# Performance work log

Hardware: AMD Instinct MI355X
Metric: run time of the kernel (lower is better)

The kernel has to match this reference:

```python
import jax, jax.numpy as jnp
import numpy as np

N = 100000
E = 1600000
DIMS = [128, 128, 64]


def _gcn_norm(edge_index, num_nodes):
    # PyG gcn_norm: add self-loops, symmetric normalization D^-1/2 (A+I) D^-1/2
    src, dst = edge_index[0], edge_index[1]
    loop = jnp.arange(num_nodes, dtype=src.dtype)
    src = jnp.concatenate([src, loop])
    dst = jnp.concatenate([dst, loop])
    deg = jax.ops.segment_sum(jnp.ones_like(src, dtype=jnp.float32), dst,
                              num_segments=num_nodes)
    dinv = jnp.where(deg > 0, jax.lax.rsqrt(deg), 0.0)
    w = dinv[src] * dinv[dst]  # [E+N]
    return src, dst, w


def _gcn_conv(x, src, dst, w, W, b):
    # transform first (cheaper when out_dim <= in_dim), then aggregate
    h = x @ W                                   # [N, out]
    msg = h[src] * w[:, None]                   # gather + scale  [E+N, out]
    out = jax.ops.segment_sum(msg, dst, num_segments=x.shape[0])
    return out + b


def setup_inputs() -> dict:
    key = jax.random.key(0)
    ks = jax.random.split(key, 6)
    x = jax.random.normal(ks[0], (N, DIMS[0]), dtype=jnp.float32)
    edge_index = jax.random.randint(ks[1], (2, E), 0, N, dtype=jnp.int64)
    # Glorot-style init for GCNConv weights, zero bias (PyG default)
    W1 = jax.random.normal(ks[2], (DIMS[0], DIMS[1]), dtype=jnp.float32) / np.sqrt(DIMS[0])
    b1 = jnp.zeros((DIMS[1],), dtype=jnp.float32)
    W2 = jax.random.normal(ks[3], (DIMS[1], DIMS[2]), dtype=jnp.float32) / np.sqrt(DIMS[1])
    b2 = jnp.zeros((DIMS[2],), dtype=jnp.float32)
    return {"x": x, "edge_index": edge_index, "W1": W1, "b1": b1, "W2": W2, "b2": b2}


def reference(x, edge_index, W1, b1, W2, b2):
    src, dst, w = _gcn_norm(edge_index, x.shape[0])
    h = _gcn_conv(x, src, dst, w, W1, b1)
    h = jax.nn.relu(h)
    # dropout is identity in eval mode (deterministic reference)
    out = _gcn_conv(h, src, dst, w, W2, b2)
    return out
```

## Files before the change

kernel.cpp:

```cpp
#include <hip/hip_runtime.h>
#include <hip/hip_fp16.h>

#define TPB 256
#define CHUNK 1024
#define EPB 4096
#define CSHIFT 8
#define AGG_BLOCKS 2048

typedef _Float16 half8 __attribute__((ext_vector_type(8)));
typedef float    f32x4 __attribute__((ext_vector_type(4)));


__global__ __launch_bounds__(256) void scanA_kernel(const int* __restrict__ cnt,
                                                    int* __restrict__ row_ptr,
                                                    int* __restrict__ chunk_sums, int n) {
    __shared__ int ls[256];
    const int t    = threadIdx.x;
    const int base = blockIdx.x * CHUNK;
    const int idx  = base + t * 4;
    int4 v = make_int4(0, 0, 0, 0);
    if (idx + 3 < n) v = *(const int4*)(cnt + idx);
    else {
        if (idx + 0 < n) v.x = cnt[idx + 0];
        if (idx + 1 < n) v.y = cnt[idx + 1];
        if (idx + 2 < n) v.z = cnt[idx + 2];
        if (idx + 3 < n) v.w = cnt[idx + 3];
    }
    int s0 = v.x, s1 = s0 + v.y, s2 = s1 + v.z, s3 = s2 + v.w;
    ls[t] = s3;
    __syncthreads();
    for (int off = 1; off < 256; off <<= 1) {
        int xv = (t >= off) ? ls[t - off] : 0;
        __syncthreads();
        ls[t] += xv;
        __syncthreads();
    }
    int excl = (t == 0) ? 0 : ls[t - 1];
    if (idx + 0 < n) row_ptr[idx + 0] = excl;
    if (idx + 1 < n) row_ptr[idx + 1] = excl + s0;
    if (idx + 2 < n) row_ptr[idx + 2] = excl + s1;
    if (idx + 3 < n) row_ptr[idx + 3] = excl + s2;
    if (t == 255) chunk_sums[blockIdx.x] = ls[255];
}

__global__ __launch_bounds__(256) void scanB_kernel(int* __restrict__ chunk_sums, int nch) {
    __shared__ int ls[256];
    const int t = threadIdx.x;
    ls[t] = (t < nch) ? chunk_sums[t] : 0;
    __syncthreads();
    for (int off = 1; off < 256; off <<= 1) {
        int xv = (t >= off) ? ls[t - off] : 0;
        __syncthreads();
        ls[t] += xv;
        __syncthreads();
    }
    if (t < nch) chunk_sums[t] = (t == 0) ? 0 : ls[t - 1];
}


__global__ __launch_bounds__(256) void hist_kernel(const int* __restrict__ dst,
                                                   int* __restrict__ hist_g,
                                                   int e, int nbc, int nblk) {
    __shared__ int hs[512];
    const int t = threadIdx.x;
    for (int i = t; i < nbc; i += 256) hs[i] = 0;
    __syncthreads();
    const int e0  = blockIdx.x * EPB;
    const int lim = min(e0 + EPB, e);
    for (int i = e0 + t; i < lim; i += 256)
        atomicAdd(&hs[dst[i] >> CSHIFT], 1);
    __syncthreads();
    for (int b = t; b < nbc; b += 256)
        hist_g[b * nblk + blockIdx.x] = hs[b];
}

__global__ __launch_bounds__(256) void partition_kernel(const int* __restrict__ src,
                                                        const int* __restrict__ dst,
                                                        const int* __restrict__ hist_scan,
                                                        const int* __restrict__ chunk_sums,
                                                        int* __restrict__ pairs,
                                                        int e, int nbc, int nblk) {
    __shared__ int  hs[512];
    __shared__ int  lscan[512];
    __shared__ int  lfill[512];
    __shared__ int  base_s[512];
    __shared__ int  ls[256];
    __shared__ int2 sp[EPB];
    const int t = threadIdx.x;
    for (int i = t; i < nbc; i += 256) { hs[i] = 0; lfill[i] = 0; }
    __syncthreads();
    const int e0  = blockIdx.x * EPB;
    const int lim = min(e0 + EPB, e);
    for (int i = e0 + t; i < lim; i += 256)
        atomicAdd(&hs[dst[i] >> CSHIFT], 1);
    __syncthreads();
    int v0 = (2 * t     < nbc) ? hs[2 * t]     : 0;
    int v1 = (2 * t + 1 < nbc) ? hs[2 * t + 1] : 0;
    ls[t] = v0 + v1;
    __syncthreads();
    for (int off = 1; off < 256; off <<= 1) {
        int xv = (t >= off) ? ls[t - off] : 0;
        __syncthreads();
        ls[t] += xv;
        __syncthreads();
    }
    int excl = (t == 0) ? 0 : ls[t - 1];
    if (2 * t     < nbc) lscan[2 * t]     = excl;
    if (2 * t + 1 < nbc) lscan[2 * t + 1] = excl + v0;
    for (int b = t; b < nbc; b += 256) {
        int hidx = b * nblk + blockIdx.x;
        base_s[b] = hist_scan[hidx] + chunk_sums[hidx >> 10];
    }
    __syncthreads();
    for (int i = e0 + t; i < lim; i += 256) {
        int d = dst[i];
        int b = d >> CSHIFT;
        int r = atomicAdd(&lfill[b], 1);
        sp[lscan[b] + r] = make_int2(src[i], d);
    }
    __syncthreads();
    const int cnt = lim - e0;
    for (int i = t; i < cnt; i += 256) {
        int2 pr = sp[i];
        int  b  = pr.y >> CSHIFT;
        pairs[base_s[b] + (i - lscan[b])] = pr.x | ((pr.y & 255) << 17);
    }
}

__global__ __launch_bounds__(256) void bucket_finalize_kernel(const int* __restrict__ pairs,
                                                              const int* __restrict__ hist_scan,
                                                              const int* __restrict__ chunk_sums,
                                                              int* __restrict__ row_ptr,
                                                              float* __restrict__ dinv,
                                                              int* __restrict__ csr_src,
                                                              int n, int e, int nbc, int nblk) {
    __shared__ int cnt_s[256];
    __shared__ int fill[256];
    __shared__ int ls[256];
    const int b   = blockIdx.x;
    const int nb0 = b << CSHIFT;
    const int t   = threadIdx.x;
    const int h0  = b * nblk;
    const int r0  = hist_scan[h0] + chunk_sums[h0 >> 10];
    int r1 = e;
    if (b + 1 < nbc) {
        const int h1 = (b + 1) * nblk;
        r1 = hist_scan[h1] + chunk_sums[h1 >> 10];
    }
    cnt_s[t] = 0;
    __syncthreads();
    for (int i = r0 + t; i < r1; i += 256)
        atomicAdd(&cnt_s[pairs[i] >> 17], 1);
    __syncthreads();
    int c = cnt_s[t];
    ls[t] = c;
    __syncthreads();
    for (int off = 1; off < 256; off <<= 1) {
        int xv = (t >= off) ? ls[t - off] : 0;
        __syncthreads();
        ls[t] += xv;
        __syncthreads();
    }
    int excl = (t == 0) ? 0 : ls[t - 1];
    int node = nb0 + t;
    if (node < n) {
        row_ptr[node] = r0 + excl;
        dinv[node]    = rsqrtf((float)(c + 1));
    }
    fill[t] = r0 + excl;
    __syncthreads();
    for (int i = r0 + t; i < r1; i += 256) {
        int pr = pairs[i];
        int p  = atomicAdd(&fill[pr >> 17], 1);
        csr_src[p] = pr & 0x1FFFF;
    }
    if (b == 0 && t == 0) row_ptr[n] = e;
}


__global__ __launch_bounds__(256) void wprep_kernel(const float* __restrict__ W1,
                                                    const float* __restrict__ W2,
                                                    _Float16* __restrict__ wf1g,
                                                    _Float16* __restrict__ wf2g) {
    const int tid = threadIdx.x;
    if (blockIdx.x == 0) {
        for (int f = tid; f < 8 * 4 * 64; f += 256) {
            int c    = f >> 8;
            int i    = (f >> 6) & 3;
            int lane = f & 63;
            int quad = lane >> 4, n = lane & 15;
            const float* wp = W1 + (size_t)(i * 32 + quad * 8) * 128 + c * 16 + n;
            half8 hv;
#pragma unroll
            for (int j = 0; j < 8; ++j) hv[j] = (_Float16)wp[(size_t)j * 128];
            ((half8*)wf1g)[f] = hv;
        }
    } else {
        for (int f = tid; f < 4 * 4 * 64; f += 256) {
            int c    = f >> 8;
            int i    = (f >> 6) & 3;
            int lane = f & 63;
            int quad = lane >> 4, n = lane & 15;
            const float* wp = W2 + (size_t)(i * 32 + quad * 8) * 64 + c * 16 + n;
            half8 hv;
#pragma unroll
            for (int j = 0; j < 8; ++j) hv[j] = (_Float16)wp[(size_t)j * 64];
            ((half8*)wf2g)[f] = hv;
        }
    }
}


template <int M, bool RELU, typename XT>
__global__ __launch_bounds__(256) void gemm_mfma_kernel(const XT* __restrict__ X,
                                                        const _Float16* __restrict__ Wfg,
                                                        const float* __restrict__ dinv,
                                                        __half* __restrict__ H, int nrows) {
    constexpr int NC = M / 16;
    __shared__ __align__(16) _Float16 Wf[NC * 4 * 64 * 8];

    const int tid = threadIdx.x;
    const uint4* wb = (const uint4*)Wfg;
    for (int f = tid; f < NC * 4 * 64; f += 256)
        ((uint4*)Wf)[f] = wb[f];
    __syncthreads();

    const int  wave = tid >> 6, lane = tid & 63;
    const int  quad = lane >> 4, n16 = lane & 15;
    const long rowbase = (long)blockIdx.x * 64 + wave * 16;

    long arow = rowbase + n16;
    const XT* xrow = X + (size_t)(arow < nrows ? arow : 0) * 128;
    half8 a[4];
    if constexpr (sizeof(XT) == 4) {
        const float4* xr = (const float4*)xrow;
#pragma unroll
        for (int i = 0; i < 4; ++i) {
            float4 x0 = xr[i * 8 + quad * 2];
            float4 x1 = xr[i * 8 + quad * 2 + 1];
            if (RELU) {
                x0.x = fmaxf(x0.x, 0.f); x0.y = fmaxf(x0.y, 0.f);
                x0.z = fmaxf(x0.z, 0.f); x0.w = fmaxf(x0.w, 0.f);
                x1.x = fmaxf(x1.x, 0.f); x1.y = fmaxf(x1.y, 0.f);
                x1.z = fmaxf(x1.z, 0.f); x1.w = fmaxf(x1.w, 0.f);
            }
            half8 hv;
            hv[0] = (_Float16)x0.x; hv[1] = (_Float16)x0.y;
            hv[2] = (_Float16)x0.z; hv[3] = (_Float16)x0.w;
            hv[4] = (_Float16)x1.x; hv[5] = (_Float16)x1.y;
            hv[6] = (_Float16)x1.z; hv[7] = (_Float16)x1.w;
            a[i] = hv;
        }
    } else {
        const half8* xr = (const half8*)xrow;
#pragma unroll
        for (int i = 0; i < 4; ++i) {
            half8 hv = xr[i * 4 + quad];
            if (RELU) {
#pragma unroll
                for (int j = 0; j < 8; ++j)
                    hv[j] = (hv[j] > (_Float16)0) ? hv[j] : (_Float16)0;
            }
            a[i] = hv;
        }
    }

    float dv[4];
#pragma unroll
    for (int r = 0; r < 4; ++r) {
        long orow = rowbase + quad * 4 + r;
        dv[r] = (orow < nrows) ? dinv[orow] : 0.f;
    }

    for (int c = 0; c < NC; ++c) {
        f32x4 acc = {0.f, 0.f, 0.f, 0.f};
#pragma unroll
        for (int i = 0; i < 4; ++i) {
            half8 b = ((const half8*)Wf)[(c * 4 + i) * 64 + lane];
            acc = __builtin_amdgcn_mfma_f32_16x16x32_f16(a[i], b, acc, 0, 0, 0);
        }
#pragma unroll
        for (int r = 0; r < 4; ++r) {
            long orow = rowbase + quad * 4 + r;
            if (orow < nrows)
                H[orow * M + c * 16 + n16] = __float2half(acc[r] * dv[r]);
        }
    }
}


__device__ __forceinline__ void add_u4(float2* a, const uint4& u) {
    float2 v0 = __half22float2(*(const __half2*)&u.x);
    float2 v1 = __half22float2(*(const __half2*)&u.y);
    float2 v2 = __half22float2(*(const __half2*)&u.z);
    float2 v3 = __half22float2(*(const __half2*)&u.w);
    a[0].x += v0.x; a[0].y += v0.y;
    a[1].x += v1.x; a[1].y += v1.y;
    a[2].x += v2.x; a[2].y += v2.y;
    a[3].x += v3.x; a[3].y += v3.y;
}


__global__ __launch_bounds__(TPB) void agg_pull128_kernel(const __half* __restrict__ hs,
                                                          const int* __restrict__ csr_src,
                                                          const int* __restrict__ row_ptr,
                                                          const float* __restrict__ dinv,
                                                          const float* __restrict__ bias,
                                                          __half* __restrict__ out, int n) {
    const int wid  = blockIdx.x * (TPB / 64) + (threadIdx.x >> 6);
    const int NW   = gridDim.x * (TPB / 64);
    const int lane = threadIdx.x & 63;
    const int q    = lane >> 4;
    const int sl   = lane & 15;
    if (wid >= n) return;
    const uint4* up   = (const uint4*)hs;
    const uint4* upsl = up + sl;

    const float4* bp = (const float4*)bias;
    const float4 bb0 = bp[2 * sl], bb1 = bp[2 * sl + 1];

    int b0 = row_ptr[wid], e0 = row_ptr[wid + 1];
    int nA = wid + NW;
    int b1 = 0, e1 = 0;
    if (nA < n) { b1 = row_ptr[nA]; e1 = row_ptr[nA + 1]; }
    int m0 = e0 - b0; if (m0 > 64) m0 = 64;
    int idx0 = (lane < m0) ? csr_src[b0 + lane] : 0;
    uint4 self0 = make_uint4(0, 0, 0, 0);
    if (q == 0) self0 = up[(size_t)wid * 16 + sl];
    float dv0 = dinv[wid];

    for (int ni = wid; ni < n; ni += NW) {
        const int n1 = ni + NW, n2 = ni + 2 * NW;
        int b2 = 0, e2 = 0;
        if (n2 < n) { b2 = row_ptr[n2]; e2 = row_ptr[n2 + 1]; }
        int idx1 = 0; uint4 self1 = make_uint4(0, 0, 0, 0); float dv1 = 0.f;
        if (n1 < n) {
            int m1 = e1 - b1; if (m1 > 64) m1 = 64;
            idx1 = (lane < m1) ? csr_src[b1 + lane] : 0;
            if (q == 0) self1 = up[(size_t)n1 * 16 + sl];
            dv1 = dinv[n1];
        }
        int m = e0 - b0; if (m > 64) m = 64;
        int sA0 = __shfl(idx0, q);
        int sA1 = __shfl(idx0, 4 + q);
        int sA2 = __shfl(idx0, 8 + q);
        int sA3 = __shfl(idx0, 12 + q);
        int sB0 = __shfl(idx0, 16 + q);
        int sB1 = __shfl(idx0, 20 + q);
        int sB2 = __shfl(idx0, 24 + q);
        int sB3 = __shfl(idx0, 28 + q);
        uint4 uA0 = upsl[(size_t)(unsigned)sA0 * 16];
        uint4 uA1 = upsl[(size_t)(unsigned)sA1 * 16];
        uint4 uA2 = upsl[(size_t)(unsigned)sA2 * 16];
        uint4 uA3 = upsl[(size_t)(unsigned)sA3 * 16];
        uint4 uB0 = upsl[(size_t)(unsigned)sB0 * 16];
        uint4 uB1 = upsl[(size_t)(unsigned)sB1 * 16];
        uint4 uB2 = upsl[(size_t)(unsigned)sB2 * 16];
        uint4 uB3 = upsl[(size_t)(unsigned)sB3 * 16];
        float2 a0[4], a1[4];
#pragma unroll
        for (int k = 0; k < 4; ++k) { a0[k] = make_float2(0.f, 0.f); a1[k] = make_float2(0.f, 0.f); }
        if (m >= 32) {
            add_u4(a0, uA0); add_u4(a1, uA1); add_u4(a0, uA2); add_u4(a1, uA3);
            add_u4(a0, uB0); add_u4(a1, uB1); add_u4(a0, uB2); add_u4(a1, uB3);
        } else {
            if (q < m)      add_u4(a0, uA0);
            if (4 + q < m)  add_u4(a1, uA1);
            if (8 + q < m)  add_u4(a0, uA2);
            if (12 + q < m) add_u4(a1, uA3);
            if (16 + q < m) add_u4(a0, uB0);
            if (20 + q < m) add_u4(a1, uB1);
            if (24 + q < m) add_u4(a0, uB2);
            if (28 + q < m) add_u4(a1, uB3);
        }
        for (int j = 32; j < m; j += 16) {
            int s0 = __shfl(idx0, j + q);
            int s1 = __shfl(idx0, j + 4 + q);
            int s2 = __shfl(idx0, j + 8 + q);
            int s3 = __shfl(idx0, j + 12 + q);
            uint4 u0 = upsl[(size_t)(unsigned)s0 * 16];
            uint4 u1 = upsl[(size_t)(unsigned)s1 * 16];
            uint4 u2 = upsl[(size_t)(unsigned)s2 * 16];
            uint4 u3 = upsl[(size_t)(unsigned)s3 * 16];
            if (j + q < m)      add_u4(a0, u0);
            if (j + 4 + q < m)  add_u4(a1, u1);
            if (j + 8 + q < m)  add_u4(a0, u2);
            if (j + 12 + q < m) add_u4(a1, u3);
        }
        for (int base = b0 + 64; base < e0; base += 64) {
            int mm = e0 - base; if (mm > 64) mm = 64;
            int idxv = (lane < mm) ? csr_src[base + lane] : 0;
            for (int j = 0; j < mm; j += 16) {
                int s0 = __shfl(idxv, j + q);
                int s1 = __shfl(idxv, j + 4 + q);
                int s2 = __shfl(idxv, j + 8 + q);
                int s3 = __shfl(idxv, j + 12 + q);
                uint4 u0 = upsl[(size_t)(unsigned)s0 * 16];
                uint4 u1 = upsl[(size_t)(unsigned)s1 * 16];
                uint4 u2 = upsl[(size_t)(unsigned)s2 * 16];
                uint4 u3 = upsl[(size_t)(unsigned)s3 * 16];
                if (j + q < mm)      add_u4(a0, u0);
                if (j + 4 + q < mm)  add_u4(a1, u1);
                if (j + 8 + q < mm)  add_u4(a0, u2);
                if (j + 12 + q < mm) add_u4(a1, u3);
            }
        }
#pragma unroll
        for (int k = 0; k < 4; ++k) { a0[k].x += a1[k].x; a0[k].y += a1[k].y; }
#pragma unroll
        for (int k = 0; k < 4; ++k) {
            a0[k].x += __shfl(a0[k].x, lane ^ 16);
            a0[k].y += __shfl(a0[k].y, lane ^ 16);
            a0[k].x += __shfl(a0[k].x, lane ^ 32);
            a0[k].y += __shfl(a0[k].y, lane ^ 32);
        }
        if (q == 0) {
            float2 v0 = __half22float2(*(const __half2*)&self0.x);
            float2 v1 = __half22float2(*(const __half2*)&self0.y);
            float2 v2 = __half22float2(*(const __half2*)&self0.z);
            float2 v3 = __half22float2(*(const __half2*)&self0.w);
            __half2 h0 = __floats2half2_rn(bb0.x + dv0 * (a0[0].x + v0.x),
                                           bb0.y + dv0 * (a0[0].y + v0.y));
            __half2 h1 = __floats2half2_rn(bb0.z + dv0 * (a0[1].x + v1.x),
                                           bb0.w + dv0 * (a0[1].y + v1.y));
            __half2 h2 = __floats2half2_rn(bb1.x + dv0 * (a0[2].x + v2.x),
                                           bb1.y + dv0 * (a0[2].y + v2.y));
            __half2 h3 = __floats2half2_rn(bb1.z + dv0 * (a0[3].x + v3.x),
                                           bb1.w + dv0 * (a0[3].y + v3.y));
            uint4 ov;
            ov.x = *(const unsigned*)&h0; ov.y = *(const unsigned*)&h1;
            ov.z = *(const unsigned*)&h2; ov.w = *(const unsigned*)&h3;
            ((uint4*)out)[(size_t)ni * 16 + sl] = ov;
        }
        b0 = b1; e0 = e1; idx0 = idx1; self0 = self1; dv0 = dv1;
        b1 = b2; e1 = e2;
    }
}


__global__ __launch_bounds__(TPB) void agg_pull64_kernel(const __half* __restrict__ hs,
                                                         const int* __restrict__ csr_src,
                                                         const int* __restrict__ row_ptr,
                                                         const float* __restrict__ dinv,
                                                         const float* __restrict__ bias,
                                                         float* __restrict__ out, int n) {
    const int wid  = blockIdx.x * (TPB / 64) + (threadIdx.x >> 6);
    const int NW   = gridDim.x * (TPB / 64);
    const int lane = threadIdx.x & 63;
    const int q    = lane >> 3;
    const int sl   = lane & 7;
    if (wid >= n) return;
    const uint4* up   = (const uint4*)hs;
    const uint4* upsl = up + sl;

    const float4* bp = (const float4*)bias;
    const float4 bb0 = bp[2 * sl], bb1 = bp[2 * sl + 1];

    int b0 = row_ptr[wid], e0 = row_ptr[wid + 1];
    int nA = wid + NW;
    int b1 = 0, e1 = 0;
    if (nA < n) { b1 = row_ptr[nA]; e1 = row_ptr[nA + 1]; }
    int m0 = e0 - b0; if (m0 > 64) m0 = 64;
    int idx0 = (lane < m0) ? csr_src[b0 + lane] : 0;
    uint4 self0 = make_uint4(0, 0, 0, 0);
    if (q == 0) self0 = up[(size_t)wid * 8 + sl];
    float dv0 = dinv[wid];

    for (int ni = wid; ni < n; ni += NW) {
        const int n1 = ni + NW, n2 = ni + 2 * NW;
        int b2 = 0, e2 = 0;
        if (n2 < n) { b2 = row_ptr[n2]; e2 = row_ptr[n2 + 1]; }
        int idx1 = 0; uint4 self1 = make_uint4(0, 0, 0, 0); float dv1 = 0.f;
        if (n1 < n) {
            int m1 = e1 - b1; if (m1 > 64) m1 = 64;
            idx1 = (lane < m1) ? csr_src[b1 + lane] : 0;
            if (q == 0) self1 = up[(size_t)n1 * 8 + sl];
            dv1 = dinv[n1];
        }
        int m = e0 - b0; if (m > 64) m = 64;
        int sA0 = __shfl(idx0, q);
        int sA1 = __shfl(idx0, 8 + q);
        int sB0 = __shfl(idx0, 16 + q);
        int sB1 = __shfl(idx0, 24 + q);
        uint4 uA0 = upsl[(size_t)(unsigned)sA0 * 8];
        uint4 uA1 = upsl[(size_t)(unsigned)sA1 * 8];
        uint4 uB0 = upsl[(size_t)(unsigned)sB0 * 8];
        uint4 uB1 = upsl[(size_t)(unsigned)sB1 * 8];
        float2 a0[4], a1[4];
#pragma unroll
        for (int k = 0; k < 4; ++k) { a0[k] = make_float2(0.f, 0.f); a1[k] = make_float2(0.f, 0.f); }
        if (m >= 32) {
            add_u4(a0, uA0); add_u4(a1, uA1); add_u4(a0, uB0); add_u4(a1, uB1);
        } else {
            if (q < m)      add_u4(a0, uA0);
            if (8 + q < m)  add_u4(a1, uA1);
            if (16 + q < m) add_u4(a0, uB0);
            if (24 + q < m) add_u4(a1, uB1);
        }
        for (int j = 32; j < m; j += 16) {
            int s0 = __shfl(idx0, j + q);
            int s1 = __shfl(idx0, j + 8 + q);
            uint4 u0 = upsl[(size_t)(unsigned)s0 * 8];
            uint4 u1 = upsl[(size_t)(unsigned)s1 * 8];
            if (j + q < m)     add_u4(a0, u0);
            if (j + 8 + q < m) add_u4(a1, u1);
        }
        for (int base = b0 + 64; base < e0; base += 64) {
            int mm = e0 - base; if (mm > 64) mm = 64;
            int idxv = (lane < mm) ? csr_src[base + lane] : 0;
            for (int j = 0; j < mm; j += 16) {
                int s0 = __shfl(idxv, j + q);
                int s1 = __shfl(idxv, j + 8 + q);
                uint4 u0 = upsl[(size_t)(unsigned)s0 * 8];
                uint4 u1 = upsl[(size_t)(unsigned)s1 * 8];
                if (j + q < mm)     add_u4(a0, u0);
                if (j + 8 + q < mm) add_u4(a1, u1);
            }
        }
#pragma unroll
        for (int k = 0; k < 4; ++k) { a0[k].x += a1[k].x; a0[k].y += a1[k].y; }
#pragma unroll
        for (int k = 0; k < 4; ++k) {
            a0[k].x += __shfl(a0[k].x, lane ^ 8);
            a0[k].y += __shfl(a0[k].y, lane ^ 8);
            a0[k].x += __shfl(a0[k].x, lane ^ 16);
            a0[k].y += __shfl(a0[k].y, lane ^ 16);
            a0[k].x += __shfl(a0[k].x, lane ^ 32);
            a0[k].y += __shfl(a0[k].y, lane ^ 32);
        }
        if (q == 0) {
            float2 v0 = __half22float2(*(const __half2*)&self0.x);
            float2 v1 = __half22float2(*(const __half2*)&self0.y);
            float2 v2 = __half22float2(*(const __half2*)&self0.z);
            float2 v3 = __half22float2(*(const __half2*)&self0.w);
            float4 o0, o1;
            o0.x = bb0.x + dv0 * (a0[0].x + v0.x);
            o0.y = bb0.y + dv0 * (a0[0].y + v0.y);
            o0.z = bb0.z + dv0 * (a0[1].x + v1.x);
            o0.w = bb0.w + dv0 * (a0[1].y + v1.y);
            o1.x = bb1.x + dv0 * (a0[2].x + v2.x);
            o1.y = bb1.y + dv0 * (a0[2].y + v2.y);
            o1.z = bb1.z + dv0 * (a0[3].x + v3.x);
            o1.w = bb1.w + dv0 * (a0[3].y + v3.y);
            ((float4*)out)[(size_t)ni * 16 + 2 * sl]     = o0;
            ((float4*)out)[(size_t)ni * 16 + 2 * sl + 1] = o1;
        }
        b0 = b1; e0 = e1; idx0 = idx1; self0 = self1; dv0 = dv1;
        b1 = b2; e1 = e2;
    }
}


extern "C" void kernel_launch(void* const* d_in, const int* in_sizes, int n_in,
                              void* d_out, int out_size, void* d_ws, size_t ws_size,
                              hipStream_t stream) {
    const float* x  = (const float*)d_in[0];
    const int*   ei = (const int*)d_in[1];
    const float* W1 = (const float*)d_in[2];
    const float* b1 = (const float*)d_in[3];
    const float* W2 = (const float*)d_in[4];
    const float* b2 = (const float*)d_in[5];
    float* out = (float*)d_out;

    const int N = in_sizes[0] / 128;
    const int E = in_sizes[1] / 2;
    const int* srcv = ei;
    const int* dstv = ei + E;

    const int NBC    = (N + 255) >> CSHIFT;
    const int NBLK_E = (E + EPB - 1) / EPB;
    const int HLEN   = NBC * NBLK_E;
    const int NCHH   = (HLEN + CHUNK - 1) / CHUNK;

    char* p = (char*)d_ws;
    int*      row_ptr    = (int*)p;      p += (((size_t)N + 64) * 4 + 63) & ~(size_t)63;
    int*      chunk_sums = (int*)p;      p += 1024;
    int*      hist       = (int*)p;      p += (((size_t)HLEN + 64) * 4 + 63) & ~(size_t)63;
    int*      csr_src    = (int*)p;      p += ((size_t)E * 4 + 63) & ~(size_t)63;
    float*    dinv       = (float*)p;    p += (((size_t)N + 64) * 4 + 63) & ~(size_t)63;
    _Float16* wf1g       = (_Float16*)p; p += 8 * 4 * 64 * 16;
    _Float16* wf2g       = (_Float16*)p; p += 4 * 4 * 64 * 16;
    __half*   hs1        = (__half*)p;   p += (size_t)N * 128 * 2;
    __half*   out1       = (__half*)p;   p += (size_t)N * 128 * 2;
    int*      pairs      = (int*)out1;
    __half*   hs2        = hs1;

    wprep_kernel<<<2, 256, 0, stream>>>(W1, W2, wf1g, wf2g);

    hist_kernel<<<NBLK_E, 256, 0, stream>>>(dstv, hist, E, NBC, NBLK_E);
    scanA_kernel<<<NCHH, 256, 0, stream>>>(hist, hist, chunk_sums, HLEN);
    scanB_kernel<<<1, 256, 0, stream>>>(chunk_sums, NCHH);
    partition_kernel<<<NBLK_E, 256, 0, stream>>>(srcv, dstv, hist, chunk_sums, pairs,
                                                 E, NBC, NBLK_E);
    bucket_finalize_kernel<<<NBC, 256, 0, stream>>>(pairs, hist, chunk_sums, row_ptr, dinv,
                                                    csr_src, N, E, NBC, NBLK_E);

    gemm_mfma_kernel<128, false, float><<<(N + 63) / 64, 256, 0, stream>>>(x, wf1g, dinv, hs1, N);
    agg_pull128_kernel<<<AGG_BLOCKS, TPB, 0, stream>>>(hs1, csr_src, row_ptr, dinv, b1, out1, N);

    gemm_mfma_kernel<64, true, _Float16><<<(N + 63) / 64, 256, 0, stream>>>(
        (const _Float16*)out1, wf2g, dinv, hs2, N);
    agg_pull64_kernel<<<AGG_BLOCKS, TPB, 0, stream>>>(hs2, csr_src, row_ptr, dinv, b2, out, N);
}
```

Measured before the change: 270.8 us.

## Fuse CSR build and first GEMM into one persistent kernel with grid barriers

Merges weight prep, histogram, scans, partition, bucket finalize and the first MFMA GEMM into a single kernel that uses software grid barriers built on global atomics. It also changes the histogram scan to a per-bucket layout, so two scan kernels become in-block scans. The aim is to remove several kernel launches and the gaps between them. In exchange the GEMM now runs on only max(NBC, NBLK_E) ≈ 391 blocks looping over tiles instead of about 1563 blocks, and the barriers assume every block is resident at once, which can deadlock if it is not.

```diff
diff --git a/kernel.cpp b/kernel.cpp
--- a/kernel.cpp
+++ b/kernel.cpp
@@ -2,7 +2,6 @@
 #include <hip/hip_fp16.h>
 
 #define TPB 256
-#define CHUNK 1024
 #define EPB 4096
 #define CSHIFT 8
 #define AGG_BLOCKS 2048
@@ -11,91 +10,23 @@
 typedef float    f32x4 __attribute__((ext_vector_type(4)));
 
 
-__global__ __launch_bounds__(256) void scanA_kernel(const int* __restrict__ cnt,
-                                                    int* __restrict__ row_ptr,
-                                                    int* __restrict__ chunk_sums, int n) {
-    __shared__ int ls[256];
-    const int t    = threadIdx.x;
-    const int base = blockIdx.x * CHUNK;
-    const int idx  = base + t * 4;
-    int4 v = make_int4(0, 0, 0, 0);
-    if (idx + 3 < n) v = *(const int4*)(cnt + idx);
-    else {
-        if (idx + 0 < n) v.x = cnt[idx + 0];
-        if (idx + 1 < n) v.y = cnt[idx + 1];
-        if (idx + 2 < n) v.z = cnt[idx + 2];
-        if (idx + 3 < n) v.w = cnt[idx + 3];
-    }
-    int s0 = v.x, s1 = s0 + v.y, s2 = s1 + v.z, s3 = s2 + v.w;
-    ls[t] = s3;
+__device__ __forceinline__ void grid_barrier(int* bar, int id, int nblk) {
     __syncthreads();
-    for (int off = 1; off < 256; off <<= 1) {
-        int xv = (t >= off) ? ls[t - off] : 0;
-        __syncthreads();
-        ls[t] += xv;
-        __syncthreads();
-    }
-    int excl = (t == 0) ? 0 : ls[t - 1];
-    if (idx + 0 < n) row_ptr[idx + 0] = excl;
-    if (idx + 1 < n) row_ptr[idx + 1] = excl + s0;
-    if (idx + 2 < n) row_ptr[idx + 2] = excl + s1;
-    if (idx + 3 < n) row_ptr[idx + 3] = excl + s2;
-    if (t == 255) chunk_sums[blockIdx.x] = ls[255];
-}
-
-__global__ __launch_bounds__(256) void scanB_kernel(int* __restrict__ chunk_sums, int nch) {
-    __shared__ int ls[256];
+    if (threadIdx.x == 0) {
+        __threadfence();
+        __hip_atomic_fetch_add(&bar[id], 1, __ATOMIC_RELEASE, __HIP_MEMORY_SCOPE_AGENT);
+        while (__hip_atomic_load(&bar[id], __ATOMIC_ACQUIRE, __HIP_MEMORY_SCOPE_AGENT) < nblk)
+            __builtin_amdgcn_s_sleep(4);
+        __threadfence();
+    }
+    __syncthreads();
+}
+
+__device__ __forceinline__ void scan512_global(int* a, int len, int* ls, int* total_out) {
     const int t = threadIdx.x;
-    ls[t] = (t < nch) ? chunk_sums[t] : 0;
-    __syncthreads();
-    for (int off = 1; off < 256; off <<= 1) {
-        int xv = (t >= off) ? ls[t - off] : 0;
-        __syncthreads();
-        ls[t] += xv;
-        __syncthreads();
-    }
-    if (t < nch) chunk_sums[t] = (t == 0) ? 0 : ls[t - 1];
-}
-
-
-__global__ __launch_bounds__(256) void hist_kernel(const int* __restrict__ dst,
-                                                   int* __restrict__ hist_g,
-                                                   int e, int nbc, int nblk) {
-    __shared__ int hs[512];
-    const int t = threadIdx.x;
-    for (int i = t; i < nbc; i += 256) hs[i] = 0;
-    __syncthreads();
-    const int e0  = blockIdx.x * EPB;
-    const int lim = min(e0 + EPB, e);
-    for (int i = e0 + t; i < lim; i += 256)
-        atomicAdd(&hs[dst[i] >> CSHIFT], 1);
-    __syncthreads();
-    for (int b = t; b < nbc; b += 256)
-        hist_g[b * nblk + blockIdx.x] = hs[b];
-}
-
-__global__ __launch_bounds__(256) void partition_kernel(const int* __restrict__ src,
-                                                        const int* __restrict__ dst,
-                                                        const int* __restrict__ hist_scan,
-                                                        const int* __restrict__ chunk_sums,
-                                                        int* __restrict__ pairs,
-                                                        int e, int nbc, int nblk) {
-    __shared__ int  hs[512];
-    __shared__ int  lscan[512];
-    __shared__ int  lfill[512];
-    __shared__ int  base_s[512];
-    __shared__ int  ls[256];
-    __shared__ int2 sp[EPB];
-    const int t = threadIdx.x;
-    for (int i = t; i < nbc; i += 256) { hs[i] = 0; lfill[i] = 0; }
-    __syncthreads();
-    const int e0  = blockIdx.x * EPB;
-    const int lim = min(e0 + EPB, e);
-    for (int i = e0 + t; i < lim; i += 256)
-        atomicAdd(&hs[dst[i] >> CSHIFT], 1);
-    __syncthreads();
-    int v0 = (2 * t     < nbc) ? hs[2 * t]     : 0;
-    int v1 = (2 * t + 1 < nbc) ? hs[2 * t + 1] : 0;
+    const int i0 = 2 * t, i1 = 2 * t + 1;
+    int v0 = (i0 < len) ? a[i0] : 0;
+    int v1 = (i1 < len) ? a[i1] : 0;
     ls[t] = v0 + v1;
     __syncthreads();
     for (int off = 1; off < 256; off <<= 1) {
@@ -105,107 +36,201 @@
         __syncthreads();
     }
     int excl = (t == 0) ? 0 : ls[t - 1];
-    if (2 * t     < nbc) lscan[2 * t]     = excl;
-    if (2 * t + 1 < nbc) lscan[2 * t + 1] = excl + v0;
-    for (int b = t; b < nbc; b += 256) {
-        int hidx = b * nblk + blockIdx.x;
-        base_s[b] = hist_scan[hidx] + chunk_sums[hidx >> 10];
-    }
+    if (i0 < len) a[i0] = excl;
+    if (i1 < len) a[i1] = excl + v0;
+    if (t == 255 && total_out) *total_out = ls[255];
     __syncthreads();
-    for (int i = e0 + t; i < lim; i += 256) {
-        int d = dst[i];
-        int b = d >> CSHIFT;
-        int r = atomicAdd(&lfill[b], 1);
-        sp[lscan[b] + r] = make_int2(src[i], d);
-    }
-    __syncthreads();
-    const int cnt = lim - e0;
-    for (int i = t; i < cnt; i += 256) {
-        int2 pr = sp[i];
-        int  b  = pr.y >> CSHIFT;
-        pairs[base_s[b] + (i - lscan[b])] = pr.x | ((pr.y & 255) << 17);
-    }
-}
-
-__global__ __launch_bounds__(256) void bucket_finalize_kernel(const int* __restrict__ pairs,
-                                                              const int* __restrict__ hist_scan,
-                                                              const int* __restrict__ chunk_sums,
-                                                              int* __restrict__ row_ptr,
-                                                              float* __restrict__ dinv,
-                                                              int* __restrict__ csr_src,
-                                                              int n, int e, int nbc, int nblk) {
-    __shared__ int cnt_s[256];
-    __shared__ int fill[256];
-    __shared__ int ls[256];
-    const int b   = blockIdx.x;
-    const int nb0 = b << CSHIFT;
-    const int t   = threadIdx.x;
-    const int h0  = b * nblk;
-    const int r0  = hist_scan[h0] + chunk_sums[h0 >> 10];
-    int r1 = e;
-    if (b + 1 < nbc) {
-        const int h1 = (b + 1) * nblk;
-        r1 = hist_scan[h1] + chunk_sums[h1 >> 10];
-    }
-    cnt_s[t] = 0;
-    __syncthreads();
-    for (int i = r0 + t; i < r1; i += 256)
-        atomicAdd(&cnt_s[pairs[i] >> 17], 1);
-    __syncthreads();
-    int c = cnt_s[t];
-    ls[t] = c;
-    __syncthreads();
-    for (int off = 1; off < 256; off <<= 1) {
-        int xv = (t >= off) ? ls[t - off] : 0;
-        __syncthreads();
-        ls[t] += xv;
-        __syncthreads();
-    }
-    int excl = (t == 0) ? 0 : ls[t - 1];
-    int node = nb0 + t;
-    if (node < n) {
-        row_ptr[node] = r0 + excl;
-        dinv[node]    = rsqrtf((float)(c + 1));
-    }
-    fill[t] = r0 + excl;
-    __syncthreads();
-    for (int i = r0 + t; i < r1; i += 256) {
-        int pr = pairs[i];
-        int p  = atomicAdd(&fill[pr >> 17], 1);
-        csr_src[p] = pr & 0x1FFFF;
-    }
-    if (b == 0 && t == 0) row_ptr[n] = e;
-}
-
-
-__global__ __launch_bounds__(256) void wprep_kernel(const float* __restrict__ W1,
-                                                    const float* __restrict__ W2,
-                                                    _Float16* __restrict__ wf1g,
-                                                    _Float16* __restrict__ wf2g) {
-    const int tid = threadIdx.x;
-    if (blockIdx.x == 0) {
-        for (int f = tid; f < 8 * 4 * 64; f += 256) {
-            int c    = f >> 8;
-            int i    = (f >> 6) & 3;
-            int lane = f & 63;
-            int quad = lane >> 4, n = lane & 15;
-            const float* wp = W1 + (size_t)(i * 32 + quad * 8) * 128 + c * 16 + n;
+}
+
+
+__global__ __launch_bounds__(256) void mega_kernel(
+    const float* __restrict__ W1, const float* __restrict__ W2,
+    _Float16* __restrict__ wf1g, _Float16* __restrict__ wf2g,
+    const int* __restrict__ src, const int* __restrict__ dst,
+    int* __restrict__ hist, int* __restrict__ chunk_sums,
+    int* __restrict__ pairs, int* __restrict__ row_ptr,
+    float* __restrict__ dinv, int* __restrict__ csr_src,
+    const float* __restrict__ X, __half* __restrict__ hs1,
+    int* __restrict__ bar,
+    int n, int e, int nbc, int nblk, int ntiles) {
+
+    __shared__ __align__(16) char smem[42496];
+    const int t = threadIdx.x;
+    const int b = blockIdx.x;
+    const int G = gridDim.x;
+
+    if (b < nblk) {
+        int* hs = (int*)smem;
+        for (int i = t; i < nbc; i += 256) hs[i] = 0;
+        __syncthreads();
+        const int e0  = b * EPB;
+        const int lim = min(e0 + EPB, e);
+        for (int i = e0 + t; i < lim; i += 256)
+            atomicAdd(&hs[dst[i] >> CSHIFT], 1);
+        __syncthreads();
+        for (int bk = t; bk < nbc; bk += 256)
+            hist[bk * nblk + b] = hs[bk];
+    }
+    if (b == 0) {
+        for (int f = t; f < 8 * 4 * 64; f += 256) {
+            int c = f >> 8, i = (f >> 6) & 3, lane = f & 63;
+            int quad = lane >> 4, nn = lane & 15;
+            const float* wp = W1 + (size_t)(i * 32 + quad * 8) * 128 + c * 16 + nn;
             half8 hv;
 #pragma unroll
             for (int j = 0; j < 8; ++j) hv[j] = (_Float16)wp[(size_t)j * 128];
             ((half8*)wf1g)[f] = hv;
         }
-    } else {
-        for (int f = tid; f < 4 * 4 * 64; f += 256) {
-            int c    = f >> 8;
-            int i    = (f >> 6) & 3;
-            int lane = f & 63;
-            int quad = lane >> 4, n = lane & 15;
-            const float* wp = W2 + (size_t)(i * 32 + quad * 8) * 64 + c * 16 + n;
+    } else if (b == 1) {
+        for (int f = t; f < 4 * 4 * 64; f += 256) {
+            int c = f >> 8, i = (f >> 6) & 3, lane = f & 63;
+            int quad = lane >> 4, nn = lane & 15;
+            const float* wp = W2 + (size_t)(i * 32 + quad * 8) * 64 + c * 16 + nn;
             half8 hv;
 #pragma unroll
             for (int j = 0; j < 8; ++j) hv[j] = (_Float16)wp[(size_t)j * 64];
             ((half8*)wf2g)[f] = hv;
+        }
+    }
+    grid_barrier(bar, 0, G);
+
+    if (b < nbc)
+        scan512_global(hist + (size_t)b * nblk, nblk, (int*)smem, &chunk_sums[b]);
+    grid_barrier(bar, 1, G);
+
+    if (b == 0)
+        scan512_global(chunk_sums, nbc, (int*)smem, nullptr);
+    grid_barrier(bar, 2, G);
+
+    if (b < nblk) {
+        int*  hs     = (int*)smem;
+        int*  lscan  = hs + 512;
+        int*  lfill  = lscan + 512;
+        int*  base_s = lfill + 512;
+        int*  ls     = base_s + 512;
+        int2* sp     = (int2*)(ls + 256);
+        for (int i = t; i < nbc; i += 256) { hs[i] = 0; lfill[i] = 0; }
+        __syncthreads();
+        const int e0  = b * EPB;
+        const int lim = min(e0 + EPB, e);
+        for (int i = e0 + t; i < lim; i += 256)
+            atomicAdd(&hs[dst[i] >> CSHIFT], 1);
+        __syncthreads();
+        int v0 = (2 * t     < nbc) ? hs[2 * t]     : 0;
+        int v1 = (2 * t + 1 < nbc) ? hs[2 * t + 1] : 0;
+        ls[t] = v0 + v1;
+        __syncthreads();
+        for (int off = 1; off < 256; off <<= 1) {
+            int xv = (t >= off) ? ls[t - off] : 0;
+            __syncthreads();
+            ls[t] += xv;
+            __syncthreads();
+        }
+        int excl = (t == 0) ? 0 : ls[t - 1];
+        if (2 * t     < nbc) lscan[2 * t]     = excl;
+        if (2 * t + 1 < nbc) lscan[2 * t + 1] = excl + v0;
+        for (int bk = t; bk < nbc; bk += 256)
+            base_s[bk] = hist[(size_t)bk * nblk + b] + chunk_sums[bk];
+        __syncthreads();
+        for (int i = e0 + t; i < lim; i += 256) {
+            int d = dst[i];
+            int bk = d >> CSHIFT;
+            int r = atomicAdd(&lfill[bk], 1);
+            sp[lscan[bk] + r] = make_int2(src[i], d);
+        }
+        __syncthreads();
+        const int cnt = lim - e0;
+        for (int i = t; i < cnt; i += 256) {
+            int2 pr = sp[i];
+            int  bk = pr.y >> CSHIFT;
+            pairs[base_s[bk] + (i - lscan[bk])] = pr.x | ((pr.y & 255) << 17);
+        }
+    }
+    grid_barrier(bar, 3, G);
+
+    if (b < nbc) {
+        int* cnt_s = (int*)smem;
+        int* fill  = cnt_s + 256;
+        int* ls    = fill + 256;
+        const int nb0 = b << CSHIFT;
+        const int r0  = hist[(size_t)b * nblk] + chunk_sums[b];
+        int r1 = e;
+        if (b + 1 < nbc) r1 = hist[(size_t)(b + 1) * nblk] + chunk_sums[b + 1];
+        cnt_s[t] = 0;
+        __syncthreads();
+        for (int i = r0 + t; i < r1; i += 256)
+            atomicAdd(&cnt_s[pairs[i] >> 17], 1);
+        __syncthreads();
+        int c = cnt_s[t];
+        ls[t] = c;
+        __syncthreads();
+        for (int off = 1; off < 256; off <<= 1) {
+            int xv = (t >= off) ? ls[t - off] : 0;
+            __syncthreads();
+            ls[t] += xv;
+            __syncthreads();
+        }
+        int excl = (t == 0) ? 0 : ls[t - 1];
+        int node = nb0 + t;
+        if (node < n) {
+            row_ptr[node] = r0 + excl;
+            dinv[node]    = rsqrtf((float)(c + 1));
+        }
+        fill[t] = r0 + excl;
+        __syncthreads();
+        for (int i = r0 + t; i < r1; i += 256) {
+            int pr = pairs[i];
+            int p  = atomicAdd(&fill[pr >> 17], 1);
+            csr_src[p] = pr & 0x1FFFF;
+        }
+        if (b == 0 && t == 0) row_ptr[n] = e;
+    }
+    grid_barrier(bar, 4, G);
+
+    {
+        _Float16* Wf = (_Float16*)smem;
+        const uint4* wb = (const uint4*)wf1g;
+        for (int f = t; f < 8 * 4 * 64; f += 256)
+            ((uint4*)Wf)[f] = wb[f];
+        __syncthreads();
+        const int wave = t >> 6, lane = t & 63;
+        const int quad = lane >> 4, n16 = lane & 15;
+        for (int tile = b; tile < ntiles; tile += G) {
+            const long rowbase = (long)tile * 64 + wave * 16;
+            long arow = rowbase + n16;
+            const float4* xr = (const float4*)(X + (size_t)(arow < n ? arow : 0) * 128);
+            half8 a[4];
+#pragma unroll
+            for (int i = 0; i < 4; ++i) {
+                float4 x0 = xr[i * 8 + quad * 2];
+                float4 x1 = xr[i * 8 + quad * 2 + 1];
+                half8 hv;
+                hv[0] = (_Float16)x0.x; hv[1] = (_Float16)x0.y;
+                hv[2] = (_Float16)x0.z; hv[3] = (_Float16)x0.w;
+                hv[4] = (_Float16)x1.x; hv[5] = (_Float16)x1.y;
+                hv[6] = (_Float16)x1.z; hv[7] = (_Float16)x1.w;
+                a[i] = hv;
+            }
+            float dv[4];
+#pragma unroll
+            for (int r = 0; r < 4; ++r) {
+                long orow = rowbase + quad * 4 + r;
+                dv[r] = (orow < n) ? dinv[orow] : 0.f;
+            }
+            for (int c = 0; c < 8; ++c) {
+                f32x4 acc = {0.f, 0.f, 0.f, 0.f};
+#pragma unroll
+                for (int i = 0; i < 4; ++i) {
+                    half8 bb = ((const half8*)Wf)[(c * 4 + i) * 64 + lane];
+                    acc = __builtin_amdgcn_mfma_f32_16x16x32_f16(a[i], bb, acc, 0, 0, 0);
+                }
+#pragma unroll
+                for (int r = 0; r < 4; ++r) {
+                    long orow = rowbase + quad * 4 + r;
+                    if (orow < n)
+                        hs1[orow * 128 + c * 16 + n16] = __float2half(acc[r] * dv[r]);
+                }
+            }
         }
     }
 }
@@ -570,32 +595,29 @@
     const int NBC    = (N + 255) >> CSHIFT;
     const int NBLK_E = (E + EPB - 1) / EPB;
     const int HLEN   = NBC * NBLK_E;
-    const int NCHH   = (HLEN + CHUNK - 1) / CHUNK;
+    const int G      = (NBC > NBLK_E) ? NBC : NBLK_E;
+    const int NTILES = (N + 63) / 64;
 
     char* p = (char*)d_ws;
     int*      row_ptr    = (int*)p;      p += (((size_t)N + 64) * 4 + 63) & ~(size_t)63;
-    int*      chunk_sums = (int*)p;      p += 1024;
+    int*      chunk_sums = (int*)p;      p += 4096;
     int*      hist       = (int*)p;      p += (((size_t)HLEN + 64) * 4 + 63) & ~(size_t)63;
     int*      csr_src    = (int*)p;      p += ((size_t)E * 4 + 63) & ~(size_t)63;
     float*    dinv       = (float*)p;    p += (((size_t)N + 64) * 4 + 63) & ~(size_t)63;
     _Float16* wf1g       = (_Float16*)p; p += 8 * 4 * 64 * 16;
     _Float16* wf2g       = (_Float16*)p; p += 4 * 4 * 64 * 16;
+    int*      bar        = (int*)p;      p += 64;
     __half*   hs1        = (__half*)p;   p += (size_t)N * 128 * 2;
     __half*   out1       = (__half*)p;   p += (size_t)N * 128 * 2;
     int*      pairs      = (int*)out1;
     __half*   hs2        = hs1;
 
-    wprep_kernel<<<2, 256, 0, stream>>>(W1, W2, wf1g, wf2g);
-
-    hist_kernel<<<NBLK_E, 256, 0, stream>>>(dstv, hist, E, NBC, NBLK_E);
-    scanA_kernel<<<NCHH, 256, 0, stream>>>(hist, hist, chunk_sums, HLEN);
-    scanB_kernel<<<1, 256, 0, stream>>>(chunk_sums, NCHH);
-    partition_kernel<<<NBLK_E, 256, 0, stream>>>(srcv, dstv, hist, chunk_sums, pairs,
-                                                 E, NBC, NBLK_E);
-    bucket_finalize_kernel<<<NBC, 256, 0, stream>>>(pairs, hist, chunk_sums, row_ptr, dinv,
-                                                    csr_src, N, E, NBC, NBLK_E);
-
-    gemm_mfma_kernel<128, false, float><<<(N + 63) / 64, 256, 0, stream>>>(x, wf1g, dinv, hs1, N);
+    hipMemsetAsync(bar, 0, 64, stream);
+
+    mega_kernel<<<G, 256, 0, stream>>>(W1, W2, wf1g, wf2g, srcv, dstv,
+                                       hist, chunk_sums, pairs, row_ptr, dinv, csr_src,
+                                       x, hs1, bar, N, E, NBC, NBLK_E, NTILES);
+
     agg_pull128_kernel<<<AGG_BLOCKS, TPB, 0, stream>>>(hs1, csr_src, row_ptr, dinv, b1, out1, N);
 
     gemm_mfma_kernel<64, true, _Float16><<<(N + 63) / 64, 256, 0, stream>>>(
```

Result: slower. 641.8 us (+137.0%).
